# Performance work log

Measured on AMD Instinct MI355X. Metric: run time of the kernel, lower is better.

## Reference

```python
import jax, jax.numpy as jnp
import numpy as np

C = 64
CQ = C // 8
CR = C // 16  # SE reduction


def _conv1x1(x, W, b):
    # x: [B,C,V,T], W: [O,C], b: [O]
    return jnp.einsum('bcvt,oc->bovt', x, W) + b[None, :, None, None]


def setup_inputs() -> dict:
    key = jax.random.key(0)
    ks = jax.random.split(key, 10)
    B, V, T = 4, 224, 224
    s = 0.05
    return {
        'x': jax.random.normal(ks[0], (B, C, V, T), jnp.float32),
        'Wq': jax.random.normal(ks[1], (CQ, C), jnp.float32) * s,
        'bq': jax.random.normal(ks[2], (CQ,), jnp.float32) * s,
        'Wk': jax.random.normal(ks[3], (CQ, C), jnp.float32) * s,
        'bk': jax.random.normal(ks[4], (CQ,), jnp.float32) * s,
        'Wv': jax.random.normal(ks[5], (C, C), jnp.float32) * s,
        'bv': jax.random.normal(ks[6], (C,), jnp.float32) * s,
        'gamma': jax.random.normal(ks[7], (), jnp.float32) * 0.5,
        'W1': jax.random.normal(ks[8], (CR, C), jnp.float32) * s,
        'W2': jax.random.normal(ks[9], (C, CR), jnp.float32) * s,
    }


def reference(x, Wq, bq, Wk, bk, Wv, bv, gamma, W1, W2):
    B, Cc, V, T = x.shape
    # ---- CrissCrossAttention (add_input=True) ----
    q = _conv1x1(x, Wq, bq)  # [B,CQ,V,T]
    k = _conv1x1(x, Wk, bk)  # [B,CQ,V,T]
    v = _conv1x1(x, Wv, bv)  # [B,C,V,T]
    # column (H) attention: energy_H[b,v,t,u] = q[b,:,v,t].k[b,:,u,t], diag -inf
    energy_H = jnp.einsum('bcvt,bcut->bvtu', q, k)
    diag = jnp.eye(V, dtype=bool)[:, None, :]  # [V,1,V]
    energy_H = jnp.where(diag[None], -jnp.inf, energy_H)
    # row (W) attention: energy_W[b,v,t,s] = q[b,:,v,t].k[b,:,v,s]
    energy_W = jnp.einsum('bcvt,bcvs->bvts', q, k)
    concate = jax.nn.softmax(jnp.concatenate([energy_H, energy_W], axis=-1), axis=-1)
    att_H = concate[..., :V]       # [B,V,T,V]
    att_W = concate[..., V:V + T]  # [B,V,T,T]
    out_H = jnp.einsum('bcut,bvtu->bcvt', v, att_H)
    out_W = jnp.einsum('bcvs,bvts->bcvt', v, att_W)
    x1 = gamma * (out_H + out_W) + x
    # ---- SELayer (mul_input=True) ----
    y = jnp.mean(x, axis=(2, 3))                # [B,C]
    y = jax.nn.relu(jnp.einsum('bc,rc->br', y, W1))
    y = jax.nn.sigmoid(jnp.einsum('br,cr->bc', y, W2))
    x2 = x * y[:, :, None, None]
    # ---- structure == 'parallel' ----
    return x1 + x2
```

## Files before the change

### kernel.cpp

```cpp
#include <hip/hip_runtime.h>
#include <math.h>

#define CC 64
#define CQv 8
#define CRv 4
#define BB 4
#define RR 224
#define TT 224
#define NN (RR*TT)
#define LOG2E 1.4426950408889634f

typedef __attribute__((ext_vector_type(8))) short short8;
typedef __attribute__((ext_vector_type(4))) float f32x4;

__device__ __forceinline__ f32x4 mfma_bf16(short8 a, short8 b, f32x4 c){
    return __builtin_amdgcn_mfma_f32_16x16x32_bf16(a, b, c, 0, 0, 0);
}

__device__ __forceinline__ ushort f2bf(float f){
    union { float f; unsigned u; } v; v.f = f;
    unsigned r = v.u + 0x7fffu + ((v.u >> 16) & 1u);
    return (ushort)(r >> 16);
}
__device__ __forceinline__ float bf2f(ushort u){
    return __uint_as_float((unsigned)u << 16);
}
__device__ __forceinline__ unsigned packbf(float a, float b){
    return __builtin_amdgcn_perm(__float_as_uint(b), __float_as_uint(a), 0x07060302u);
}
__device__ __forceinline__ int vswz(int row, int uslot){
    return (uslot ^ (row & 7) ^ ((row >> 3) & 7)) << 4;
}

__global__ __launch_bounds__(256) void k_qkv(
    const float* __restrict__ x,
    const float* __restrict__ Wq, const float* __restrict__ bq,
    const float* __restrict__ Wk, const float* __restrict__ bk,
    const float* __restrict__ Wv, const float* __restrict__ bv,
    ushort* __restrict__ qB, ushort* __restrict__ kB, ushort* __restrict__ vB,
    float* __restrict__ partial)
{
    const int tid = threadIdx.x;
    const int w = tid >> 6, l = tid & 63, l15 = l & 15, lg = l >> 4;
    const int blk = blockIdx.x;
    const int b = blk / 196, pb = blk - b*196;
    const int n0 = pb*256;
    const float* xb = x + (size_t)b*CC*NN;

    short8 afr[5][2];
#pragma unroll
    for (int ot = 0; ot < 5; ++ot) {
        int oo = ot*16 + l15;
        const float* wr = (oo < 8) ? (Wq + oo*64)
                        : (oo < 16) ? (Wk + (oo-8)*64)
                                    : (Wv + (oo-16)*64);
        float scl = (oo >= 8 && oo < 16) ? LOG2E : 1.0f;
#pragma unroll
        for (int ks = 0; ks < 2; ++ks) {
            const float* p = wr + ks*32 + lg*8;
            float4 w0 = *(const float4*)p, w1 = *(const float4*)(p+4);
            short8 f;
            f[0]=f2bf(w0.x*scl); f[1]=f2bf(w0.y*scl); f[2]=f2bf(w0.z*scl); f[3]=f2bf(w0.w*scl);
            f[4]=f2bf(w1.x*scl); f[5]=f2bf(w1.y*scl); f[6]=f2bf(w1.z*scl); f[7]=f2bf(w1.w*scl);
            afr[ot][ks] = f;
        }
    }
    f32x4 binit[5];
#pragma unroll
    for (int ot = 0; ot < 5; ++ot) {
        const float* bp;
        float scl = 1.0f;
        if (ot == 0) { bp = (lg < 2) ? (bq + lg*4) : (bk + (lg-2)*4); if (lg >= 2) scl = LOG2E; }
        else           bp = bv + (ot-1)*16 + lg*4;
        float4 bb4 = *(const float4*)bp;
        binit[ot] = (f32x4){bb4.x*scl, bb4.y*scl, bb4.z*scl, bb4.w*scl};
    }

    float msum[16];
#pragma unroll
    for (int i = 0; i < 16; ++i) msum[i] = 0.f;

#pragma unroll
    for (int j = 0; j < 4; ++j) {
        int n = n0 + (w*4 + j)*16 + l15;
        short8 bfr[2];
#pragma unroll
        for (int ks = 0; ks < 2; ++ks) {
            const float* xp = xb + (size_t)(ks*32 + lg*8)*NN + n;
            short8 f;
#pragma unroll
            for (int e = 0; e < 8; ++e) {
                float xv = xp[(size_t)e*NN];
                f[e] = f2bf(xv);
                msum[ks*8 + e] += xv;
            }
            bfr[ks] = f;
        }
#pragma unroll
        for (int ot = 0; ot < 5; ++ot) {
            f32x4 acc = binit[ot];
            acc = mfma_bf16(afr[ot][0], bfr[0], acc);
            acc = mfma_bf16(afr[ot][1], bfr[1], acc);
            ushort4 pk;
            pk.x = f2bf(acc[0]); pk.y = f2bf(acc[1]);
            pk.z = f2bf(acc[2]); pk.w = f2bf(acc[3]);
            if (ot == 0) {
                ushort* dst = (lg < 2) ? (qB + ((size_t)b*NN + n)*8 + lg*4)
                                       : (kB + ((size_t)b*NN + n)*8 + (lg-2)*4);
                *(ushort4*)dst = pk;
            } else {
                int oc = (ot-1)*16 + lg*4;
                *(ushort4*)(vB + ((size_t)b*NN + n)*64 + oc) = pk;
            }
        }
    }

#pragma unroll
    for (int i = 0; i < 16; ++i) {
        float s = msum[i];
        s += __shfl_xor(s, 1); s += __shfl_xor(s, 2);
        s += __shfl_xor(s, 4); s += __shfl_xor(s, 8);
        msum[i] = s;
    }
    __shared__ float msums[4][4][16];
    if (l15 == 0) {
#pragma unroll
        for (int i = 0; i < 16; ++i) msums[w][lg][i] = msum[i];
    }
    __syncthreads();
    if (tid < 64) {
        int c = tid;
        int lgi = (c >> 3) & 3, ii = (c >> 5)*8 + (c & 7);
        float t = msums[0][lgi][ii] + msums[1][lgi][ii] + msums[2][lgi][ii] + msums[3][lgi][ii];
        partial[(size_t)blk*64 + c] = t;
    }
}

__global__ __launch_bounds__(256) void k_tq(const uint4* __restrict__ qs, const uint4* __restrict__ ks,
                                            uint4* __restrict__ qd, uint4* __restrict__ kd)
{
    __shared__ uint4 tile[32][33];
    int z = blockIdx.z;
    int b = z & 3;
    const uint4* sp = ((z >= 4) ? ks : qs) + (size_t)b*NN;
    uint4*       dp = ((z >= 4) ? kd : qd) + (size_t)b*NN;
    int t0 = blockIdx.x*32, r0 = blockIdx.y*32;
    int tx = threadIdx.x & 31, ty = threadIdx.x >> 5;
#pragma unroll
    for (int j = 0; j < 4; ++j) { int lr = ty + 8*j; tile[lr][tx] = sp[(size_t)(r0+lr)*224 + t0 + tx]; }
    __syncthreads();
#pragma unroll
    for (int j = 0; j < 4; ++j) { int lt = ty + 8*j; dp[(size_t)(t0+lt)*224 + r0 + tx] = tile[tx][lt]; }
}

__global__ __launch_bounds__(256, 3) void k_pv(const ushort* __restrict__ qA, const ushort* __restrict__ kA,
                                               const ushort* __restrict__ qB, const ushort* __restrict__ kB,
                                               const ushort* __restrict__ vB,
                                               ushort* __restrict__ outA, ushort* __restrict__ outB,
                                               float* __restrict__ ZHt, float* __restrict__ ZWt)
{
    __shared__ __align__(16) ushort Vt[64*256];
    __shared__ __align__(16) ushort Kh[224*8];

    const int tid = threadIdx.x;
    const int bid = blockIdx.x;
    const bool HM = bid < BB*224;
    const int blk = HM ? bid : bid - BB*224;
    const int b = blk / 224, o = blk - b*224;
    const ushort* Qsrc = (HM ? qA : qB) + (size_t)blk*1792;
    const ushort* Ksrc = (HM ? kA : kB) + (size_t)blk*1792;
    ushort* op = (HM ? outA : outB) + (size_t)blk*14336;
    float*  Zt = (HM ? ZHt : ZWt) + (size_t)blk*224;

    {
        const uint4* vbase = (const uint4*)vB;
        for (int gi = tid; gi < 448; gi += 256) {
            int ublk = gi >> 3, sub = gi & 7;
            int u0 = ublk << 2;
            size_t base, stride;
            if (HM) { base = ((size_t)b*NN + (size_t)u0*224 + o)*8 + sub; stride = 1792; }
            else    { base = ((size_t)blk*224 + u0)*8 + sub;              stride = 8;    }
            uint4 r0 = vbase[base], r1 = vbase[base+stride], r2 = vbase[base+2*stride], r3 = vbase[base+3*stride];
            const ushort* p0 = (const ushort*)&r0;
            const ushort* p1 = (const ushort*)&r1;
            const ushort* p2 = (const ushort*)&r2;
            const ushort* p3 = (const ushort*)&r3;
            int ks   = ublk >> 3;
            int th   = (ublk >> 2) & 1;
            int quad = ublk & 3;
            int half = th * 8;
#pragma unroll
            for (int j = 0; j < 8; ++j) {
                int c = sub*8 + j;
                ushort4 col; col.x = p0[j]; col.y = p1[j]; col.z = p2[j]; col.w = p3[j];
                *(ushort4*)((char*)Vt + c*512 + vswz(c, ks*4 + quad) + half) = col;
            }
        }
    }
    if (tid < 224) ((uint4*)Kh)[tid] = ((const uint4*)Ksrc)[tid];
    __syncthreads();

    const int w = tid >> 6, l = tid & 63;
    const int l15 = l & 15, lg = l >> 4;
    const short8 zfr = {0,0,0,0,0,0,0,0};
    const f32x4 zacc = {0.f,0.f,0.f,0.f};

#pragma unroll 1
    for (int p = 0; p < 2; ++p) {
        const int ch0 = w + p*8;
        const int ch1 = ch0 + 4;
        const bool do1 = (ch1 < 14);
        short8 qf0 = zfr, qf1 = zfr;
        if (lg == 0) {
            qf0 = *(const short8*)(Qsrc + (size_t)(ch0*16 + l15)*8);
            if (do1) qf1 = *(const short8*)(Qsrc + (size_t)(ch1*16 + l15)*8);
        }
        f32x4 acc00 = zacc, acc01 = zacc, acc02 = zacc, acc03 = zacc;
        f32x4 acc10 = zacc, acc11 = zacc, acc12 = zacc, acc13 = zacc;
        float zs0 = 0.f, zs1 = 0.f;
#pragma unroll 1
        for (int ks = 0; ks < 7; ++ks) {
            short8 kf0 = *(const short8*)(Kh + (size_t)(ks*32 + l15)*8);
            short8 kf1 = *(const short8*)(Kh + (size_t)(ks*32 + 16 + l15)*8);
            f32x4 e00 = mfma_bf16(kf0, qf0, zacc);
            f32x4 e01 = mfma_bf16(kf1, qf0, zacc);
            f32x4 e10 = mfma_bf16(kf0, qf1, zacc);
            f32x4 e11 = mfma_bf16(kf1, qf1, zacc);
            float a00[4], a01[4], a10[4], a11[4];
#pragma unroll
            for (int g = 0; g < 4; ++g) {
                a00[g] = __builtin_amdgcn_exp2f(e00[g]);
                a01[g] = __builtin_amdgcn_exp2f(e01[g]);
                a10[g] = __builtin_amdgcn_exp2f(e10[g]);
                a11[g] = __builtin_amdgcn_exp2f(e11[g]);
            }
            if (HM && (ch0 >> 1) == ks) {
                if ((ch0 & 1) == 0) {
#pragma unroll
                    for (int g = 0; g < 4; ++g) if (lg*4 + g == l15) a00[g] = 0.f;
                } else {
#pragma unroll
                    for (int g = 0; g < 4; ++g) if (lg*4 + g == l15) a01[g] = 0.f;
                }
            }
            if (HM && do1 && (ch1 >> 1) == ks) {
                if ((ch1 & 1) == 0) {
#pragma unroll
                    for (int g = 0; g < 4; ++g) if (lg*4 + g == l15) a10[g] = 0.f;
                } else {
#pragma unroll
                    for (int g = 0; g < 4; ++g) if (lg*4 + g == l15) a11[g] = 0.f;
                }
            }
            zs0 += ((a00[0]+a00[1]) + (a00[2]+a00[3])) + ((a01[0]+a01[1]) + (a01[2]+a01[3]));
            zs1 += ((a10[0]+a10[1]) + (a10[2]+a10[3])) + ((a11[0]+a11[1]) + (a11[2]+a11[3]));
            int4 i0, i1;
            i0.x = (int)packbf(a00[0], a00[1]); i0.y = (int)packbf(a00[2], a00[3]);
            i0.z = (int)packbf(a01[0], a01[1]); i0.w = (int)packbf(a01[2], a01[3]);
            i1.x = (int)packbf(a10[0], a10[1]); i1.y = (int)packbf(a10[2], a10[3]);
            i1.z = (int)packbf(a11[0], a11[1]); i1.w = (int)packbf(a11[2], a11[3]);
            short8 af0 = *(short8*)&i0;
            short8 af1 = *(short8*)&i1;
            {
                short8 vf0 = *(const short8*)((const char*)Vt + (size_t)(l15)*512       + vswz(l15,      ks*4 + lg));
                short8 vf1 = *(const short8*)((const char*)Vt + (size_t)(16 + l15)*512  + vswz(16 + l15, ks*4 + lg));
                short8 vf2 = *(const short8*)((const char*)Vt + (size_t)(32 + l15)*512  + vswz(32 + l15, ks*4 + lg));
                short8 vf3 = *(const short8*)((const char*)Vt + (size_t)(48 + l15)*512  + vswz(48 + l15, ks*4 + lg));
                acc00 = mfma_bf16(vf0, af0, acc00);
                acc10 = mfma_bf16(vf0, af1, acc10);
                acc01 = mfma_bf16(vf1, af0, acc01);
                acc11 = mfma_bf16(vf1, af1, acc11);
                acc02 = mfma_bf16(vf2, af0, acc02);
                acc12 = mfma_bf16(vf2, af1, acc12);
                acc03 = mfma_bf16(vf3, af0, acc03);
                acc13 = mfma_bf16(vf3, af1, acc13);
            }
        }
        zs0 += __shfl_xor(zs0, 16);
        zs0 += __shfl_xor(zs0, 32);
        zs1 += __shfl_xor(zs1, 16);
        zs1 += __shfl_xor(zs1, 32);
        if (lg == 0) {
            Zt[ch0*16 + l15] = zs0;
            if (do1) Zt[ch1*16 + l15] = zs1;
        }
        {
            int pos = ch0*16 + l15;
            f32x4 av[4] = {acc00, acc01, acc02, acc03};
#pragma unroll
            for (int ct = 0; ct < 4; ++ct) {
                ushort4 pk;
                pk.x = f2bf(av[ct][0]); pk.y = f2bf(av[ct][1]);
                pk.z = f2bf(av[ct][2]); pk.w = f2bf(av[ct][3]);
                *(ushort4*)(op + (size_t)pos*64 + ct*16 + lg*4) = pk;
            }
        }
        if (do1) {
            int pos = ch1*16 + l15;
            f32x4 av[4] = {acc10, acc11, acc12, acc13};
#pragma unroll
            for (int ct = 0; ct < 4; ++ct) {
                ushort4 pk;
                pk.x = f2bf(av[ct][0]); pk.y = f2bf(av[ct][1]);
                pk.z = f2bf(av[ct][2]); pk.w = f2bf(av[ct][3]);
                *(ushort4*)(op + (size_t)pos*64 + ct*16 + lg*4) = pk;
            }
        }
    }
}

__global__ __launch_bounds__(256) void k_aux(const float* __restrict__ ZHt, const float* __restrict__ ZWt,
                                             const float* __restrict__ gammap,
                                             const float* __restrict__ partial,
                                             const float* __restrict__ W1, const float* __restrict__ W2,
                                             float* __restrict__ Zi, float* __restrict__ y2)
{
    const int blk = blockIdx.x;
    if (blk < 196) {
        __shared__ float tile[32][33];
        int b = blk / 49, rem = blk - b*49;
        int t0 = (rem % 7)*32, v0 = (rem / 7)*32;
        int tx = threadIdx.x & 31, ty = threadIdx.x >> 5;
        float g = gammap[0];
#pragma unroll
        for (int j = 0; j < 4; ++j) {
            int tl = ty + 8*j;
            tile[tl][tx] = ZHt[((size_t)(b*224 + t0 + tl))*224 + v0 + tx];
        }
        __syncthreads();
#pragma unroll
        for (int j = 0; j < 4; ++j) {
            int vl = ty + 8*j;
            size_t i = ((size_t)(b*224 + v0 + vl))*224 + t0 + tx;
            float zs = tile[tx][vl] + ZWt[i];
            Zi[i] = g * __builtin_amdgcn_rcpf(zs);
        }
    } else {
        __shared__ float mean_s[4][64];
        int tid = threadIdx.x;
        int b = tid >> 6, c = tid & 63;
        float s = 0.f;
        for (int i = 0; i < 196; ++i) s += partial[((size_t)(b*196 + i))*64 + c];
        mean_s[b][c] = s * (1.0f/NN);
        __syncthreads();
        float h[CRv];
#pragma unroll
        for (int j = 0; j < CRv; ++j) {
            float t = 0.f;
#pragma unroll
            for (int cc = 0; cc < CC; ++cc) t += W1[j*CC + cc] * mean_s[b][cc];
            h[j] = fmaxf(t, 0.f);
        }
        float s2 = 0.f;
#pragma unroll
        for (int j = 0; j < CRv; ++j) s2 += W2[c*CRv + j] * h[j];
        y2[tid] = 1.f/(1.f + __expf(-s2));
    }
}

__global__ __launch_bounds__(256) void k_final(const float* __restrict__ x,
                                               const ushort* __restrict__ outA,
                                               const ushort* __restrict__ outB,
                                               const float* __restrict__ Zi,
                                               const float* __restrict__ y2,
                                               float* __restrict__ out)
{
    __shared__ float Ls[2][16][65];
    __shared__ float sc[64];
    const int b = blockIdx.z;
    const int v0 = blockIdx.y*16, t0 = blockIdx.x*16;
    const int tid = threadIdx.x;
    if (tid < 64) sc[tid] = 1.f + y2[b*64 + tid];

    const int tl = tid >> 4, cg = tid & 15;
    const int tg = tid & 3, cw = tid >> 2;

    const ushort* pA = outA + (size_t)b*NN*64;
    const ushort* pB = outB + (size_t)b*NN*64;
    __syncthreads();

    for (int vl = 0; vl < 16; ++vl) {
        const int v = v0 + vl;
        const int buf = vl & 1;
        {
            const ushort* a4 = pA + ((size_t)(t0 + tl)*224 + v)*64 + cg*4;
            const ushort* b4 = pB + ((size_t)v*224 + (t0 + tl))*64 + cg*4;
            uint2 ra = *(const uint2*)a4;
            uint2 rb = *(const uint2*)b4;
            const ushort* qa = (const ushort*)&ra;
            const ushort* qb = (const ushort*)&rb;
            float zi = Zi[(size_t)b*NN + (size_t)v*224 + t0 + tl];
#pragma unroll
            for (int j = 0; j < 4; ++j)
                Ls[buf][tl][cg*4 + j] = (bf2f(qa[j]) + bf2f(qb[j])) * zi;
        }
        __syncthreads();
        {
            float s = sc[cw];
            size_t idx = (size_t)(b*64 + cw)*NN + (size_t)v*224 + t0 + tg*4;
            float4 xv = *(const float4*)(x + idx);
            float4 o;
            o.x = xv.x*s + Ls[buf][tg*4+0][cw];
            o.y = xv.y*s + Ls[buf][tg*4+1][cw];
            o.z = xv.z*s + Ls[buf][tg*4+2][cw];
            o.w = xv.w*s + Ls[buf][tg*4+3][cw];
            *(float4*)(out + idx) = o;
        }
    }
}

extern "C" void kernel_launch(void* const* d_in, const int* in_sizes, int n_in,
                              void* d_out, int out_size, void* d_ws, size_t ws_size,
                              hipStream_t stream)
{
    const float* x  = (const float*)d_in[0];
    const float* Wq = (const float*)d_in[1];
    const float* bq = (const float*)d_in[2];
    const float* Wk = (const float*)d_in[3];
    const float* bk = (const float*)d_in[4];
    const float* Wv = (const float*)d_in[5];
    const float* bv = (const float*)d_in[6];
    const float* gm = (const float*)d_in[7];
    const float* W1 = (const float*)d_in[8];
    const float* W2 = (const float*)d_in[9];
    float* out = (float*)d_out;

    constexpr size_t QSZ = (size_t)BB*NN*CQv;
    constexpr size_t VSZ = (size_t)BB*NN*CC;
    constexpr size_t SSZ = (size_t)BB*NN;

    ushort* qB = (ushort*)d_ws;
    ushort* kB = qB + QSZ;
    ushort* vB = kB + QSZ;
    ushort* qA = vB + VSZ;
    ushort* kA = qA + QSZ;
    ushort* outA = kA + QSZ;
    ushort* outB = outA + VSZ;
    float*  ZHt = (float*)(outB + VSZ);
    float*  ZWt = ZHt + SSZ;
    float*  Zi  = ZWt + SSZ;
    float*  partial = Zi + SSZ;
    float*  y2 = partial + (size_t)BB*196*64;
    (void)ws_size; (void)in_sizes; (void)n_in; (void)out_size;

    k_qkv<<<BB*196, 256, 0, stream>>>(x, Wq, bq, Wk, bk, Wv, bv, qB, kB, vB, partial);
    k_tq<<<dim3(7,7,8), 256, 0, stream>>>((const uint4*)qB, (const uint4*)kB, (uint4*)qA, (uint4*)kA);

    k_pv<<<2*BB*224, 256, 0, stream>>>(qA, kA, qB, kB, vB, outA, outB, ZHt, ZWt);
    k_aux<<<197, 256, 0, stream>>>(ZHt, ZWt, gm, partial, W1, W2, Zi, y2);

    k_final<<<dim3(14,14,BB), 256, 0, stream>>>(x, outA, outB, Zi, y2, out);
}
```

Baseline: 109.9 us.

## Remove k_aux kernel: fold SE into k_tq, normalizer into k_final, prefetch K

Drops the separate k_aux launch. The SE-layer squeeze/excite computation moves into an extra z-slice of the transpose kernel, and the softmax normalizer (gamma / (ZH+ZW)) is computed inline in k_final, so the Zi buffer and one kernel launch with its global round trip go away. The K fragments in k_pv are also software-prefetched one iteration ahead to hide load latency. In exchange, k_final now reads ZHt with a strided, uncoalesced column access, and the extra z-slice in k_tq launches 49 blocks of which 48 exit immediately.

```diff
diff --git a/kernel.cpp b/kernel.cpp
--- a/kernel.cpp
+++ b/kernel.cpp
@@ -137,10 +137,36 @@
 }
 
 __global__ __launch_bounds__(256) void k_tq(const uint4* __restrict__ qs, const uint4* __restrict__ ks,
-                                            uint4* __restrict__ qd, uint4* __restrict__ kd)
+                                            uint4* __restrict__ qd, uint4* __restrict__ kd,
+                                            const float* __restrict__ partial,
+                                            const float* __restrict__ W1, const float* __restrict__ W2,
+                                            float* __restrict__ y2)
 {
+    int z = blockIdx.z;
+    if (z == 8) {
+        if (blockIdx.x || blockIdx.y) return;
+        __shared__ float mean_s[4][64];
+        int tid = threadIdx.x;
+        int b = tid >> 6, c = tid & 63;
+        float s = 0.f;
+        for (int i = 0; i < 196; ++i) s += partial[((size_t)(b*196 + i))*64 + c];
+        mean_s[b][c] = s * (1.0f/NN);
+        __syncthreads();
+        float h[CRv];
+#pragma unroll
+        for (int j = 0; j < CRv; ++j) {
+            float t = 0.f;
+#pragma unroll
+            for (int cc = 0; cc < CC; ++cc) t += W1[j*CC + cc] * mean_s[b][cc];
+            h[j] = fmaxf(t, 0.f);
+        }
+        float s2 = 0.f;
+#pragma unroll
+        for (int j = 0; j < CRv; ++j) s2 += W2[c*CRv + j] * h[j];
+        y2[tid] = 1.f/(1.f + __expf(-s2));
+        return;
+    }
     __shared__ uint4 tile[32][33];
-    int z = blockIdx.z;
     int b = z & 3;
     const uint4* sp = ((z >= 4) ? ks : qs) + (size_t)b*NN;
     uint4*       dp = ((z >= 4) ? kd : qd) + (size_t)b*NN;
@@ -218,14 +244,17 @@
         f32x4 acc00 = zacc, acc01 = zacc, acc02 = zacc, acc03 = zacc;
         f32x4 acc10 = zacc, acc11 = zacc, acc12 = zacc, acc13 = zacc;
         float zs0 = 0.f, zs1 = 0.f;
+        short8 kf0c = *(const short8*)(Kh + (size_t)(l15)*8);
+        short8 kf1c = *(const short8*)(Kh + (size_t)(16 + l15)*8);
 #pragma unroll 1
         for (int ks = 0; ks < 7; ++ks) {
-            short8 kf0 = *(const short8*)(Kh + (size_t)(ks*32 + l15)*8);
-            short8 kf1 = *(const short8*)(Kh + (size_t)(ks*32 + 16 + l15)*8);
-            f32x4 e00 = mfma_bf16(kf0, qf0, zacc);
-            f32x4 e01 = mfma_bf16(kf1, qf0, zacc);
-            f32x4 e10 = mfma_bf16(kf0, qf1, zacc);
-            f32x4 e11 = mfma_bf16(kf1, qf1, zacc);
+            f32x4 e00 = mfma_bf16(kf0c, qf0, zacc);
+            f32x4 e01 = mfma_bf16(kf1c, qf0, zacc);
+            f32x4 e10 = mfma_bf16(kf0c, qf1, zacc);
+            f32x4 e11 = mfma_bf16(kf1c, qf1, zacc);
+            int ksn = (ks == 6) ? 0 : ks + 1;
+            short8 kf0n = *(const short8*)(Kh + (size_t)(ksn*32 + l15)*8);
+            short8 kf1n = *(const short8*)(Kh + (size_t)(ksn*32 + 16 + l15)*8);
             float a00[4], a01[4], a10[4], a11[4];
 #pragma unroll
             for (int g = 0; g < 4; ++g) {
@@ -275,6 +304,7 @@
                 acc03 = mfma_bf16(vf3, af0, acc03);
                 acc13 = mfma_bf16(vf3, af1, acc13);
             }
+            kf0c = kf0n; kf1c = kf1n;
         }
         zs0 += __shfl_xor(zs0, 16);
         zs0 += __shfl_xor(zs0, 32);
@@ -309,59 +339,12 @@
     }
 }
 
-__global__ __launch_bounds__(256) void k_aux(const float* __restrict__ ZHt, const float* __restrict__ ZWt,
-                                             const float* __restrict__ gammap,
-                                             const float* __restrict__ partial,
-                                             const float* __restrict__ W1, const float* __restrict__ W2,
-                                             float* __restrict__ Zi, float* __restrict__ y2)
-{
-    const int blk = blockIdx.x;
-    if (blk < 196) {
-        __shared__ float tile[32][33];
-        int b = blk / 49, rem = blk - b*49;
-        int t0 = (rem % 7)*32, v0 = (rem / 7)*32;
-        int tx = threadIdx.x & 31, ty = threadIdx.x >> 5;
-        float g = gammap[0];
-#pragma unroll
-        for (int j = 0; j < 4; ++j) {
-            int tl = ty + 8*j;
-            tile[tl][tx] = ZHt[((size_t)(b*224 + t0 + tl))*224 + v0 + tx];
-        }
-        __syncthreads();
-#pragma unroll
-        for (int j = 0; j < 4; ++j) {
-            int vl = ty + 8*j;
-            size_t i = ((size_t)(b*224 + v0 + vl))*224 + t0 + tx;
-            float zs = tile[tx][vl] + ZWt[i];
-            Zi[i] = g * __builtin_amdgcn_rcpf(zs);
-        }
-    } else {
-        __shared__ float mean_s[4][64];
-        int tid = threadIdx.x;
-        int b = tid >> 6, c = tid & 63;
-        float s = 0.f;
-        for (int i = 0; i < 196; ++i) s += partial[((size_t)(b*196 + i))*64 + c];
-        mean_s[b][c] = s * (1.0f/NN);
-        __syncthreads();
-        float h[CRv];
-#pragma unroll
-        for (int j = 0; j < CRv; ++j) {
-            float t = 0.f;
-#pragma unroll
-            for (int cc = 0; cc < CC; ++cc) t += W1[j*CC + cc] * mean_s[b][cc];
-            h[j] = fmaxf(t, 0.f);
-        }
-        float s2 = 0.f;
-#pragma unroll
-        for (int j = 0; j < CRv; ++j) s2 += W2[c*CRv + j] * h[j];
-        y2[tid] = 1.f/(1.f + __expf(-s2));
-    }
-}
-
 __global__ __launch_bounds__(256) void k_final(const float* __restrict__ x,
                                                const ushort* __restrict__ outA,
                                                const ushort* __restrict__ outB,
-                                               const float* __restrict__ Zi,
+                                               const float* __restrict__ ZHt,
+                                               const float* __restrict__ ZWt,
+                                               const float* __restrict__ gammap,
                                                const float* __restrict__ y2,
                                                float* __restrict__ out)
 {
@@ -370,6 +353,7 @@
     const int b = blockIdx.z;
     const int v0 = blockIdx.y*16, t0 = blockIdx.x*16;
     const int tid = threadIdx.x;
+    const float g = gammap[0];
     if (tid < 64) sc[tid] = 1.f + y2[b*64 + tid];
 
     const int tl = tid >> 4, cg = tid & 15;
@@ -389,7 +373,9 @@
             uint2 rb = *(const uint2*)b4;
             const ushort* qa = (const ushort*)&ra;
             const ushort* qb = (const ushort*)&rb;
-            float zi = Zi[(size_t)b*NN + (size_t)v*224 + t0 + tl];
+            float zh = ZHt[((size_t)(b*224 + t0 + tl))*224 + v];
+            float zw = ZWt[((size_t)(b*224 + v))*224 + t0 + tl];
+            float zi = g * __builtin_amdgcn_rcpf(zh + zw);
 #pragma unroll
             for (int j = 0; j < 4; ++j)
                 Ls[buf][tl][cg*4 + j] = (bf2f(qa[j]) + bf2f(qb[j])) * zi;
@@ -438,16 +424,15 @@
     ushort* outB = outA + VSZ;
     float*  ZHt = (float*)(outB + VSZ);
     float*  ZWt = ZHt + SSZ;
-    float*  Zi  = ZWt + SSZ;
-    float*  partial = Zi + SSZ;
+    float*  partial = ZWt + SSZ;
     float*  y2 = partial + (size_t)BB*196*64;
     (void)ws_size; (void)in_sizes; (void)n_in; (void)out_size;
 
     k_qkv<<<BB*196, 256, 0, stream>>>(x, Wq, bq, Wk, bk, Wv, bv, qB, kB, vB, partial);
-    k_tq<<<dim3(7,7,8), 256, 0, stream>>>((const uint4*)qB, (const uint4*)kB, (uint4*)qA, (uint4*)kA);
+    k_tq<<<dim3(7,7,9), 256, 0, stream>>>((const uint4*)qB, (const uint4*)kB, (uint4*)qA, (uint4*)kA,
+                                          partial, W1, W2, y2);
 
     k_pv<<<2*BB*224, 256, 0, stream>>>(qA, kA, qB, kB, vB, outA, outB, ZHt, ZWt);
-    k_aux<<<197, 256, 0, stream>>>(ZHt, ZWt, gm, partial, W1, W2, Zi, y2);
-
-    k_final<<<dim3(14,14,BB), 256, 0, stream>>>(x, outA, outB, Zi, y2, out);
-}
+
+    k_final<<<dim3(14,14,BB), 256, 0, stream>>>(x, outA, outB, ZHt, ZWt, gm, y2, out);
+}
```

Measured after the change: 108.4 us (median of 3 runs). Within noise of the previous version (-1.4%).
